# Kernel optimization log

Hardware: AMD Instinct MI355X
Metric: run time of the kernel (lower is better)

The kernel has to match this reference:

```python
import jax, jax.numpy as jnp
import numpy as np
from jax import lax

WINDOW_SIZE = 11
SIGMA = 1.5
C1 = 0.01 ** 2
C2 = 0.03 ** 2


def _gaussian_window(channels: int) -> jnp.ndarray:
    x = np.arange(WINDOW_SIZE)
    g = np.exp(-((x - WINDOW_SIZE // 2) ** 2) / (2.0 * SIGMA ** 2))
    g = g / g.sum()
    w2d = np.outer(g, g).astype(np.float32)  # [k,k]
    # depthwise kernel: [C, 1, k, k] in OIHW with feature_group_count=C
    return jnp.asarray(np.tile(w2d[None, None], (channels, 1, 1, 1)))


def _depthwise_blur(x: jnp.ndarray, window: jnp.ndarray) -> jnp.ndarray:
    pad = WINDOW_SIZE // 2
    return lax.conv_general_dilated(
        x, window,
        window_strides=(1, 1),
        padding=[(pad, pad), (pad, pad)],
        feature_group_count=x.shape[1],
        dimension_numbers=("NCHW", "OIHW", "NCHW"),
    )


def setup_inputs() -> dict:
    key = jax.random.key(0)
    k1, k2 = jax.random.split(key)
    pred = jax.random.normal(k1, (16, 3, 512, 512), dtype=jnp.float32)
    target = jax.random.normal(k2, (16, 3, 512, 512), dtype=jnp.float32)
    return {"pred": pred, "target": target}


def reference(pred, target):
    pred = (pred + 1.0) / 2.0
    target = (target + 1.0) / 2.0
    channels = pred.shape[1]
    window = _gaussian_window(channels)

    mu_p = _depthwise_blur(pred, window)
    mu_t = _depthwise_blur(target, window)
    mu_p_sq = mu_p * mu_p
    mu_t_sq = mu_t * mu_t
    mu_pt = mu_p * mu_t

    sigma_p_sq = _depthwise_blur(pred * pred, window) - mu_p_sq
    sigma_t_sq = _depthwise_blur(target * target, window) - mu_t_sq
    sigma_pt = _depthwise_blur(pred * target, window) - mu_pt

    ssim_map = ((2.0 * mu_pt + C1) * (2.0 * sigma_pt + C2)) / (
        (mu_p_sq + mu_t_sq + C1) * (sigma_p_sq + sigma_t_sq + C2)
    )
    return 1.0 - jnp.mean(ssim_map)
```

## Files before the change

### kernel.cpp

```cpp
#include <hip/hip_runtime.h>
#include <math.h>


#define IMG 512
#define TW 64
#define TH 16
#define NT 4
#define GXD 8
#define GYD 8
#define GZD 48
#define NB (GXD * GYD * GZD)
#define VBS 88
#define C1c 0.0001f
#define C2c 0.0009f
#define NTOTAL 12582912.0f

typedef short bf16x8 __attribute__((ext_vector_type(8)));
typedef float f32x4 __attribute__((ext_vector_type(4)));

struct GaussB { unsigned short gb[11]; };

__device__ __forceinline__ unsigned int pkbf(float a, float b) {
    return __builtin_amdgcn_perm(__float_as_uint(b), __float_as_uint(a),
                                 0x07060302u);
}

__device__ __forceinline__ void barrier_lds_only() {
    __builtin_amdgcn_s_waitcnt(0xc07f);
    __builtin_amdgcn_s_barrier();
}

__device__ __forceinline__ void load_col8(const float* __restrict__ pbase,
                                          const float* __restrict__ tbase,
                                          int gx, int gy0, bool xin,
                                          float* pv, float* tv)
{
    const bool ok = xin & (gy0 >= 0) & (gy0 <= IMG - 8);
    if (ok) {
        const float* pp = pbase + gy0 * IMG + gx;
        const float* tp = tbase + gy0 * IMG + gx;
        #pragma unroll
        for (int j = 0; j < 8; ++j) {
            pv[j] = pp[j * IMG];
            tv[j] = tp[j * IMG];
        }
    } else {
        #pragma unroll
        for (int j = 0; j < 8; ++j) {
            int gy = gy0 + j;
            bool in = xin && ((unsigned)gy < (unsigned)IMG);
            int idx = in ? (gy * IMG + gx) : 0;
            float a = pbase[idx];
            float b = tbase[idx];
            pv[j] = in ? a : 0.0f;
            tv[j] = in ? b : 0.0f;
        }
    }
}

template <bool USE_ATOMIC>
__global__ __launch_bounds__(320, 8) void ssim_main(
    const float* __restrict__ pred,
    const float* __restrict__ target,
    float* __restrict__ sink,
    GaussB gwb)
{
    __shared__ unsigned short Wmat[16][32];
    __shared__ unsigned short vb[5][16][VBS];
    __shared__ float red[5];

    const int tid  = threadIdx.x;
    const int w    = tid >> 6;
    const int lane = tid & 63;
    const int quad = lane >> 4;
    const int n16  = lane & 15;
    const int tx0  = blockIdx.x * TW;
    const int tyb  = blockIdx.y * (TH * NT);
    const float* __restrict__ pbase = pred   + (size_t)blockIdx.z * (IMG * IMG);
    const float* __restrict__ tbase = target + (size_t)blockIdx.z * (IMG * IMG);

    for (int idx = tid; idx < 512; idx += 320) {
        int i = idx >> 5, k = idx & 31, d = k - i;
        Wmat[i][k] = (d >= 0 && d <= 10) ? gwb.gb[d] : 0;
    }
    __syncthreads();
    const bf16x8 wfrag = *(const bf16x8*)&Wmat[n16][quad * 8];

    const int gx  = tx0 - 5 + 16 * w + n16;
    const bool xin = (unsigned)gx < (unsigned)IMG;
    const int k0  = quad * 8;
    const int vcol = 16 * w + 4 * quad;
    const f32x4 z = {0.0f, 0.0f, 0.0f, 0.0f};

    float pv[2][8], tv[2][8];
    load_col8(pbase, tbase, gx, tyb - 5 + k0, xin, pv[0], tv[0]);

    float lsum = 0.0f;

    #pragma unroll
    for (int i = 0; i < NT; ++i) {
        const int cur = i & 1, nxt = cur ^ 1;
        if (i + 1 < NT)
            load_col8(pbase, tbase, gx, tyb + TH * (i + 1) - 5 + k0, xin,
                      pv[nxt], tv[nxt]);

        float ps[8], ts[8];
        #pragma unroll
        for (int j = 0; j < 8; ++j) {
            ps[j] = fmaf(pv[cur][j], 0.5f, 0.5f);
            ts[j] = fmaf(tv[cur][j], 0.5f, 0.5f);
        }
        #pragma unroll
        for (int ch = 0; ch < 5; ++ch) {
            union { bf16x8 v; unsigned int u[4]; } f;
            #pragma unroll
            for (int h = 0; h < 4; ++h) {
                float a0, a1;
                if      (ch == 0) { a0 = ps[2*h];            a1 = ps[2*h+1]; }
                else if (ch == 1) { a0 = ts[2*h];            a1 = ts[2*h+1]; }
                else if (ch == 2) { a0 = ps[2*h]*ps[2*h];    a1 = ps[2*h+1]*ps[2*h+1]; }
                else if (ch == 3) { a0 = ts[2*h]*ts[2*h];    a1 = ts[2*h+1]*ts[2*h+1]; }
                else              { a0 = ps[2*h]*ts[2*h];    a1 = ps[2*h+1]*ts[2*h+1]; }
                f.u[h] = pkbf(a0, a1);
            }
            f32x4 d = __builtin_amdgcn_mfma_f32_16x16x32_bf16(f.v, wfrag, z, 0, 0, 0);
            union { ushort4 s; unsigned int u[2]; } pk;
            pk.u[0] = pkbf(d[0], d[1]);
            pk.u[1] = pkbf(d[2], d[3]);
            *(ushort4*)&vb[ch][n16][vcol] = pk.s;
        }
        barrier_lds_only();

        if (w < 4) {
            f32x4 r[5];
            #pragma unroll
            for (int ch = 0; ch < 5; ++ch) {
                bf16x8 a = *(const bf16x8*)&vb[ch][n16][16 * w + 8 * quad];
                r[ch] = __builtin_amdgcn_mfma_f32_16x16x32_bf16(a, wfrag, z, 0, 0, 0);
            }
            #pragma unroll
            for (int j = 0; j < 4; ++j) {
                float mp = r[0][j], mt = r[1][j];
                float mp2 = mp * mp, mt2 = mt * mt, mpt = mp * mt;
                float sig_p  = r[2][j] - mp2;
                float sig_t  = r[3][j] - mt2;
                float sig_pt = r[4][j] - mpt;
                float num = (2.0f * mpt + C1c) * (2.0f * sig_pt + C2c);
                float den = (mp2 + mt2 + C1c) * (sig_p + sig_t + C2c);
                lsum = fmaf(num, __builtin_amdgcn_rcpf(den), lsum);
            }
        }
        __syncthreads();
    }

    #pragma unroll
    for (int off = 32; off > 0; off >>= 1)
        lsum += __shfl_down(lsum, off, 64);
    if (lane == 0) red[w] = lsum;
    __syncthreads();
    if (tid == 0) {
        float s = red[0] + red[1] + red[2] + red[3];
        if (USE_ATOMIC) {
            atomicAdd(sink, s);
        } else {
            int bid = blockIdx.x + GXD * (blockIdx.y + GYD * blockIdx.z);
            sink[bid] = s;
        }
    }
}

__global__ __launch_bounds__(256) void ssim_reduce(const float* __restrict__ partials,
                                                   float* __restrict__ out)
{
    __shared__ float red[4];
    const int tid = threadIdx.x;
    float s = 0.0f;
    const float4* p4 = (const float4*)partials;
    #pragma unroll
    for (int j = 0; j < NB / 1024; ++j) {
        float4 v = p4[tid + 256 * j];
        s += v.x + v.y + v.z + v.w;
    }
    #pragma unroll
    for (int off = 32; off > 0; off >>= 1)
        s += __shfl_down(s, off, 64);
    if ((tid & 63) == 0) red[tid >> 6] = s;
    __syncthreads();
    if (tid == 0)
        out[0] = 1.0f - (red[0] + red[1] + red[2] + red[3]) / NTOTAL;
}

__global__ void ssim_zero(float* accum) { accum[0] = 0.0f; }
__global__ void ssim_final(const float* accum, float* out) {
    out[0] = 1.0f - accum[0] / NTOTAL;
}

extern "C" void kernel_launch(void* const* d_in, const int* in_sizes, int n_in,
                              void* d_out, int out_size, void* d_ws, size_t ws_size,
                              hipStream_t stream) {
    const float* pred   = (const float*)d_in[0];
    const float* target = (const float*)d_in[1];
    float* out = (float*)d_out;

    GaussB gwb;
    double vals[11], s = 0.0;
    for (int i = 0; i < 11; ++i) {
        double d = (double)i - 5.0;
        vals[i] = exp(-(d * d) / (2.0 * 1.5 * 1.5));
        s += vals[i];
    }
    for (int i = 0; i < 11; ++i) {
        float f = (float)(vals[i] / s);
        unsigned int u;
        __builtin_memcpy(&u, &f, 4);
        unsigned int rounded = (u + 0x7FFFu + ((u >> 16) & 1u)) >> 16;
        gwb.gb[i] = (unsigned short)rounded;
    }

    dim3 grid(GXD, GYD, GZD);
    if (ws_size >= (size_t)NB * sizeof(float)) {
        float* partials = (float*)d_ws;
        ssim_main<false><<<grid, 320, 0, stream>>>(pred, target, partials, gwb);
        ssim_reduce<<<1, 256, 0, stream>>>(partials, out);
    } else {
        float* accum = (float*)d_ws;
        ssim_zero<<<1, 1, 0, stream>>>(accum);
        ssim_main<true><<<grid, 320, 0, stream>>>(pred, target, accum, gwb);
        ssim_final<<<1, 1, 0, stream>>>(accum, out);
    }
}
```

Baseline: 159.7 us.

## Process one 16-row tile per block, drop in-block prefetch loop, use packed float2 math

```diff
diff --git a/kernel.cpp b/kernel.cpp
--- a/kernel.cpp
+++ b/kernel.cpp
@@ -5,9 +5,8 @@
 #define IMG 512
 #define TW 64
 #define TH 16
-#define NT 4
 #define GXD 8
-#define GYD 8
+#define GYD 32
 #define GZD 48
 #define NB (GXD * GYD * GZD)
 #define VBS 88
@@ -17,6 +16,7 @@
 
 typedef short bf16x8 __attribute__((ext_vector_type(8)));
 typedef float f32x4 __attribute__((ext_vector_type(4)));
+typedef float f32x2 __attribute__((ext_vector_type(2)));
 
 struct GaussB { unsigned short gb[11]; };
 
@@ -25,41 +25,8 @@
                                  0x07060302u);
 }
 
-__device__ __forceinline__ void barrier_lds_only() {
-    __builtin_amdgcn_s_waitcnt(0xc07f);
-    __builtin_amdgcn_s_barrier();
-}
-
-__device__ __forceinline__ void load_col8(const float* __restrict__ pbase,
-                                          const float* __restrict__ tbase,
-                                          int gx, int gy0, bool xin,
-                                          float* pv, float* tv)
-{
-    const bool ok = xin & (gy0 >= 0) & (gy0 <= IMG - 8);
-    if (ok) {
-        const float* pp = pbase + gy0 * IMG + gx;
-        const float* tp = tbase + gy0 * IMG + gx;
-        #pragma unroll
-        for (int j = 0; j < 8; ++j) {
-            pv[j] = pp[j * IMG];
-            tv[j] = tp[j * IMG];
-        }
-    } else {
-        #pragma unroll
-        for (int j = 0; j < 8; ++j) {
-            int gy = gy0 + j;
-            bool in = xin && ((unsigned)gy < (unsigned)IMG);
-            int idx = in ? (gy * IMG + gx) : 0;
-            float a = pbase[idx];
-            float b = tbase[idx];
-            pv[j] = in ? a : 0.0f;
-            tv[j] = in ? b : 0.0f;
-        }
-    }
-}
-
 template <bool USE_ATOMIC>
-__global__ __launch_bounds__(320, 8) void ssim_main(
+__global__ __launch_bounds__(320, 6) void ssim_main(
     const float* __restrict__ pred,
     const float* __restrict__ target,
     float* __restrict__ sink,
@@ -75,7 +42,7 @@
     const int quad = lane >> 4;
     const int n16  = lane & 15;
     const int tx0  = blockIdx.x * TW;
-    const int tyb  = blockIdx.y * (TH * NT);
+    const int ty0  = blockIdx.y * TH;
     const float* __restrict__ pbase = pred   + (size_t)blockIdx.z * (IMG * IMG);
     const float* __restrict__ tbase = target + (size_t)blockIdx.z * (IMG * IMG);
 
@@ -86,71 +53,97 @@
     __syncthreads();
     const bf16x8 wfrag = *(const bf16x8*)&Wmat[n16][quad * 8];
 
-    const int gx  = tx0 - 5 + 16 * w + n16;
+    const int gx   = tx0 - 5 + 16 * w + n16;
     const bool xin = (unsigned)gx < (unsigned)IMG;
-    const int k0  = quad * 8;
+    const int k0   = quad * 8;
+    const int gy0  = ty0 - 5 + k0;
     const int vcol = 16 * w + 4 * quad;
     const f32x4 z = {0.0f, 0.0f, 0.0f, 0.0f};
 
-    float pv[2][8], tv[2][8];
-    load_col8(pbase, tbase, gx, tyb - 5 + k0, xin, pv[0], tv[0]);
+    float pv[8], tv[8];
+    {
+        const bool ok = xin & (gy0 >= 0) & (gy0 <= IMG - 8);
+        if (ok) {
+            const float* pp = pbase + gy0 * IMG + gx;
+            const float* tp = tbase + gy0 * IMG + gx;
+            #pragma unroll
+            for (int j = 0; j < 8; ++j) {
+                pv[j] = pp[j * IMG];
+                tv[j] = tp[j * IMG];
+            }
+        } else {
+            #pragma unroll
+            for (int j = 0; j < 8; ++j) {
+                int gy = gy0 + j;
+                bool in = xin && ((unsigned)gy < (unsigned)IMG);
+                int idx = in ? (gy * IMG + gx) : 0;
+                float a = pbase[idx];
+                float b = tbase[idx];
+                pv[j] = in ? a : 0.0f;
+                tv[j] = in ? b : 0.0f;
+            }
+        }
+    }
+
+    const f32x2 halfv = {0.5f, 0.5f};
+    f32x2 p2[4], t2[4];
+    #pragma unroll
+    for (int h = 0; h < 4; ++h) {
+        f32x2 pr = {pv[2*h], pv[2*h+1]};
+        f32x2 tr = {tv[2*h], tv[2*h+1]};
+        p2[h] = pr * halfv + halfv;
+        t2[h] = tr * halfv + halfv;
+    }
+    #pragma unroll
+    for (int ch = 0; ch < 5; ++ch) {
+        union { bf16x8 v; unsigned int u[4]; } f;
+        #pragma unroll
+        for (int h = 0; h < 4; ++h) {
+            f32x2 q;
+            if      (ch == 0) q = p2[h];
+            else if (ch == 1) q = t2[h];
+            else if (ch == 2) q = p2[h] * p2[h];
+            else if (ch == 3) q = t2[h] * t2[h];
+            else              q = p2[h] * t2[h];
+            f.u[h] = pkbf(q.x, q.y);
+        }
+        f32x4 d = __builtin_amdgcn_mfma_f32_16x16x32_bf16(f.v, wfrag, z, 0, 0, 0);
+        union { ushort4 s; unsigned int u[2]; } pk;
+        pk.u[0] = pkbf(d[0], d[1]);
+        pk.u[1] = pkbf(d[2], d[3]);
+        *(ushort4*)&vb[ch][n16][vcol] = pk.s;
+    }
+    __syncthreads();
 
     float lsum = 0.0f;
-
-    #pragma unroll
-    for (int i = 0; i < NT; ++i) {
-        const int cur = i & 1, nxt = cur ^ 1;
-        if (i + 1 < NT)
-            load_col8(pbase, tbase, gx, tyb + TH * (i + 1) - 5 + k0, xin,
-                      pv[nxt], tv[nxt]);
-
-        float ps[8], ts[8];
-        #pragma unroll
-        for (int j = 0; j < 8; ++j) {
-            ps[j] = fmaf(pv[cur][j], 0.5f, 0.5f);
-            ts[j] = fmaf(tv[cur][j], 0.5f, 0.5f);
-        }
+    if (w < 4) {
+        f32x4 r[5];
         #pragma unroll
         for (int ch = 0; ch < 5; ++ch) {
-            union { bf16x8 v; unsigned int u[4]; } f;
-            #pragma unroll
-            for (int h = 0; h < 4; ++h) {
-                float a0, a1;
-                if      (ch == 0) { a0 = ps[2*h];            a1 = ps[2*h+1]; }
-                else if (ch == 1) { a0 = ts[2*h];            a1 = ts[2*h+1]; }
-                else if (ch == 2) { a0 = ps[2*h]*ps[2*h];    a1 = ps[2*h+1]*ps[2*h+1]; }
-                else if (ch == 3) { a0 = ts[2*h]*ts[2*h];    a1 = ts[2*h+1]*ts[2*h+1]; }
-                else              { a0 = ps[2*h]*ts[2*h];    a1 = ps[2*h+1]*ts[2*h+1]; }
-                f.u[h] = pkbf(a0, a1);
-            }
-            f32x4 d = __builtin_amdgcn_mfma_f32_16x16x32_bf16(f.v, wfrag, z, 0, 0, 0);
-            union { ushort4 s; unsigned int u[2]; } pk;
-            pk.u[0] = pkbf(d[0], d[1]);
-            pk.u[1] = pkbf(d[2], d[3]);
-            *(ushort4*)&vb[ch][n16][vcol] = pk.s;
-        }
-        barrier_lds_only();
-
-        if (w < 4) {
-            f32x4 r[5];
-            #pragma unroll
-            for (int ch = 0; ch < 5; ++ch) {
-                bf16x8 a = *(const bf16x8*)&vb[ch][n16][16 * w + 8 * quad];
-                r[ch] = __builtin_amdgcn_mfma_f32_16x16x32_bf16(a, wfrag, z, 0, 0, 0);
-            }
-            #pragma unroll
-            for (int j = 0; j < 4; ++j) {
-                float mp = r[0][j], mt = r[1][j];
-                float mp2 = mp * mp, mt2 = mt * mt, mpt = mp * mt;
-                float sig_p  = r[2][j] - mp2;
-                float sig_t  = r[3][j] - mt2;
-                float sig_pt = r[4][j] - mpt;
-                float num = (2.0f * mpt + C1c) * (2.0f * sig_pt + C2c);
-                float den = (mp2 + mt2 + C1c) * (sig_p + sig_t + C2c);
-                lsum = fmaf(num, __builtin_amdgcn_rcpf(den), lsum);
-            }
-        }
-        __syncthreads();
+            bf16x8 a = *(const bf16x8*)&vb[ch][n16][16 * w + 8 * quad];
+            r[ch] = __builtin_amdgcn_mfma_f32_16x16x32_bf16(a, wfrag, z, 0, 0, 0);
+        }
+        const f32x2 twov = {2.0f, 2.0f};
+        const f32x2 c1v  = {C1c, C1c};
+        const f32x2 c2v  = {C2c, C2c};
+        #pragma unroll
+        for (int jj = 0; jj < 2; ++jj) {
+            f32x2 mp  = {r[0][2*jj], r[0][2*jj+1]};
+            f32x2 mt  = {r[1][2*jj], r[1][2*jj+1]};
+            f32x2 epp = {r[2][2*jj], r[2][2*jj+1]};
+            f32x2 ett = {r[3][2*jj], r[3][2*jj+1]};
+            f32x2 ept = {r[4][2*jj], r[4][2*jj+1]};
+            f32x2 mp2 = mp * mp;
+            f32x2 mt2 = mt * mt;
+            f32x2 mpt = mp * mt;
+            f32x2 sp_ = epp - mp2;
+            f32x2 st_ = ett - mt2;
+            f32x2 spt = ept - mpt;
+            f32x2 num = (mpt * twov + c1v) * (spt * twov + c2v);
+            f32x2 den = (mp2 + mt2 + c1v) * (sp_ + st_ + c2v);
+            lsum = fmaf(num.x, __builtin_amdgcn_rcpf(den.x), lsum);
+            lsum = fmaf(num.y, __builtin_amdgcn_rcpf(den.y), lsum);
+        }
     }
 
     #pragma unroll
```

Result: faster. 137.3 us (-14.0%).
